# Optimization experiments

Hardware: AMD Instinct MI355X
Metric: run time of the kernel (lower is better)

## Reference

```python
import jax, jax.numpy as jnp
import numpy as np

DIM_IN, DIM_H, DIM_OUT = 1024, 512, 256
E, T, B = 8, 4, 16384


def setup_inputs() -> dict:
    key = jax.random.key(0)
    ks = jax.random.split(key, 8)
    s1 = 1.0 / np.sqrt(DIM_IN)
    s2 = 1.0 / np.sqrt(DIM_H)
    x = jax.random.normal(ks[0], (B, DIM_IN), dtype=jnp.float32)
    # stacked expert params: layer1 [E, H, IN], layer2 [E, OUT, H]
    W1 = jax.random.uniform(ks[1], (E, DIM_H, DIM_IN), jnp.float32, -s1, s1)
    b1 = jax.random.uniform(ks[2], (E, DIM_H), jnp.float32, -s1, s1)
    W2 = jax.random.uniform(ks[3], (E, DIM_OUT, DIM_H), jnp.float32, -s2, s2)
    b2 = jax.random.uniform(ks[4], (E, DIM_OUT), jnp.float32, -s2, s2)
    # gate params: [T, E, IN]
    Wg = jax.random.uniform(ks[5], (T, E, DIM_IN), jnp.float32, -s1, s1)
    bg = jax.random.uniform(ks[6], (T, E), jnp.float32, -s1, s1)
    return {"x": x, "W1": W1, "b1": b1, "W2": W2, "b2": b2, "Wg": Wg, "bg": bg}


def reference(x, W1, b1, W2, b2, Wg, bg):
    # Experts: Linear+ReLU, Linear+ReLU (dropout=0 / eval mode)
    h = jax.nn.relu(jnp.einsum('bi,ehi->beh', x, W1) + b1)          # [B,E,H]
    feats = jax.nn.relu(jnp.einsum('beh,edh->bed', h, W2) + b2)     # [B,E,D]
    # Gates: softmax over experts, one gate per task
    logits = jnp.einsum('bi,tei->bte', x, Wg) + bg                  # [B,T,E]
    w = jax.nn.softmax(logits, axis=-1)                             # [B,T,E]
    # Weighted combine: einsum('bde,be->bd') per task
    out = jnp.einsum('bed,bte->tbd', feats, w)                      # [T,B,D]
    return out
```

## Files before the change

kernel.cpp:

```cpp
#include <hip/hip_runtime.h>


typedef __attribute__((ext_vector_type(8))) __bf16 bf16x8;
typedef __attribute__((ext_vector_type(4))) float f32x4;

__device__ __forceinline__ unsigned short f2bf(float f) {
  union { float f; unsigned int i; } x;
  x.f = f;
  unsigned int r = x.i + 0x7FFFu + ((x.i >> 16) & 1u);
  return (unsigned short)(r >> 16);
}

__device__ __forceinline__ void gload_lds16(const unsigned short* g, unsigned short* l) {
  __builtin_amdgcn_global_load_lds(
      (const __attribute__((address_space(1))) void*)g,
      (__attribute__((address_space(3))) void*)l, 16, 0, 0);
}

__global__ void cvt_k(const float* __restrict__ in, unsigned short* __restrict__ out, int n4) {
  int i = blockIdx.x * blockDim.x + threadIdx.x;
  if (i >= n4) return;
  float4 v = ((const float4*)in)[i];
  ushort4 o;
  o.x = f2bf(v.x); o.y = f2bf(v.y); o.z = f2bf(v.z); o.w = f2bf(v.w);
  ((ushort4*)out)[i] = o;
}

__global__ __launch_bounds__(256) void gates_k(
    const unsigned short* __restrict__ xb,
    const unsigned short* __restrict__ Wgb,
    const float* __restrict__ bg,
    float* __restrict__ gw)
{
  const int lane = threadIdx.x & 63;
  const int wid = threadIdx.x >> 6;
  const int wgid = blockIdx.x * 4 + wid;
  const int brow = wgid * 16;
  const int l15 = lane & 15, lhi = lane >> 4;

  f32x4 acc0 = {0.f, 0.f, 0.f, 0.f};
  f32x4 acc1 = {0.f, 0.f, 0.f, 0.f};
  for (int k0 = 0; k0 < 1024; k0 += 32) {
    bf16x8 a  = *(const bf16x8*)&xb[(size_t)(brow + l15) * 1024 + k0 + lhi * 8];
    bf16x8 b0 = *(const bf16x8*)&Wgb[(size_t)l15 * 1024 + k0 + lhi * 8];
    bf16x8 b1 = *(const bf16x8*)&Wgb[(size_t)(16 + l15) * 1024 + k0 + lhi * 8];
    acc0 = __builtin_amdgcn_mfma_f32_16x16x32_bf16(a, b0, acc0, 0, 0, 0);
    acc1 = __builtin_amdgcn_mfma_f32_16x16x32_bf16(a, b1, acc1, 0, 0, 0);
  }
  const float bg0 = bg[l15];
  const float bg1 = bg[16 + l15];
#pragma unroll
  for (int r = 0; r < 4; ++r) {
    float v0 = acc0[r] + bg0;
    float v1 = acc1[r] + bg1;
    float m0 = v0, m1 = v1;
#pragma unroll
    for (int d = 1; d <= 4; d <<= 1) {
      m0 = fmaxf(m0, __shfl_xor(m0, d));
      m1 = fmaxf(m1, __shfl_xor(m1, d));
    }
    float e0 = __expf(v0 - m0), e1 = __expf(v1 - m1);
    float s0 = e0, s1 = e1;
#pragma unroll
    for (int d = 1; d <= 4; d <<= 1) {
      s0 += __shfl_xor(s0, d);
      s1 += __shfl_xor(s1, d);
    }
    int b = brow + lhi * 4 + r;
    gw[(size_t)b * 32 + l15]      = e0 / s0;
    gw[(size_t)b * 32 + 16 + l15] = e1 / s1;
  }
}

template <bool RELU>
__global__ __launch_bounds__(512, 2) void gemm256(
    const unsigned short* __restrict__ A, int lda, int aZ,
    const unsigned short* __restrict__ B,
    const float* __restrict__ bias,
    unsigned short* __restrict__ C, int ldc, int cZ,
    int tilesN, int N, int K)
{
  extern __shared__ char smem_raw[];
  unsigned short* lds = (unsigned short*)smem_raw;
  char* ldsb = (char*)smem_raw;

  const int tid = threadIdx.x;
  const int lane = tid & 63, wid = tid >> 6;
  const int wr = wid >> 2, wc = wid & 3;
  const int l15 = lane & 15, lhi = lane >> 4;

  const int nwg = gridDim.x;
  const int cpx = nwg >> 3;
  const int wg = blockIdx.x;
  const int swz = (wg & 7) * cpx + (wg >> 3);
  const int rt = swz / tilesN, ct = swz - rt * tilesN;
  const int brow = rt * 256, bcol = ct * 256;
  const int e = blockIdx.z;

  const unsigned short* Ab = A + (size_t)e * aZ + (size_t)brow * lda;
  const unsigned short* Bb = B + (size_t)e * N * K + (size_t)bcol * K;
  const float* biasb = bias + (size_t)e * N;
  unsigned short* Cb = C + (size_t)e * cZ;

  const int NT = K >> 6;
  const int NI = NT >> 1;

  const int trow = tid >> 3;
  const int cg8 = (((tid & 7) ^ (trow & 7)) << 3);

  const int axor = (l15 & 7) << 4;
  const int koff0 = (lhi << 4) ^ axor;
  const int koff1 = (64 + (lhi << 4)) ^ axor;

  const char* pA0 = ldsb + wr * 16384 + l15 * 128 + koff0;
  const char* pA1 = ldsb + wr * 16384 + l15 * 128 + koff1;
  const char* pB0 = ldsb + 65536 + wc * 8192 + l15 * 128 + koff0;
  const char* pB1 = ldsb + 65536 + wc * 8192 + l15 * 128 + koff1;

  f32x4 bias4[4];
#pragma unroll
  for (int nf = 0; nf < 4; ++nf)
    bias4[nf] = *(const f32x4*)&biasb[bcol + wc * 64 + nf * 16 + lhi * 4];

  const f32x4 zero = {0.f, 0.f, 0.f, 0.f};
  f32x4 acc[8][4];
#pragma unroll
  for (int m = 0; m < 8; ++m)
#pragma unroll
    for (int n = 0; n < 4; ++n) acc[m][n] = zero;

  auto STAGE_A = [&](int slot, int t, int u) {
    gload_lds16(Ab + (size_t)(u * 64 + trow) * lda + (t * 64 + cg8),
                lds + slot * 16384 + u * 4096 + wid * 512);
  };
  auto STAGE_B = [&](int slot, int t, int u) {
    gload_lds16(Bb + (size_t)(u * 64 + trow) * K + (t * 64 + cg8),
                lds + 32768 + slot * 16384 + u * 4096 + wid * 512);
  };

#pragma unroll
  for (int u = 0; u < 4; ++u) STAGE_B(0, 0, u);
#pragma unroll
  for (int u = 0; u < 4; ++u) STAGE_A(0, 0, u);
  asm volatile("s_waitcnt vmcnt(0)" ::: "memory");
  __builtin_amdgcn_s_barrier();

  auto ktile = [&](int slot, int tn, bool stageNext) {
    bf16x8 af[4][2], bfr[4][2];
#pragma unroll
    for (int mi = 0; mi < 4; ++mi) {
      af[mi][0] = *(const bf16x8*)(pA0 + slot * 32768 + mi * 2048);
      af[mi][1] = *(const bf16x8*)(pA1 + slot * 32768 + mi * 2048);
    }
#pragma unroll
    for (int n = 0; n < 2; ++n) {
      bfr[n][0] = *(const bf16x8*)(pB0 + slot * 32768 + n * 2048);
      bfr[n][1] = *(const bf16x8*)(pB1 + slot * 32768 + n * 2048);
    }
    if (stageNext) { STAGE_B(slot ^ 1, tn, 0); STAGE_B(slot ^ 1, tn, 1); }
    __builtin_amdgcn_s_barrier();
    __builtin_amdgcn_s_setprio(1);
#pragma unroll
    for (int kk = 0; kk < 2; ++kk)
#pragma unroll
      for (int mi = 0; mi < 4; ++mi)
#pragma unroll
        for (int n = 0; n < 2; ++n)
          acc[mi][n] = __builtin_amdgcn_mfma_f32_16x16x32_bf16(bfr[n][kk], af[mi][kk], acc[mi][n], 0, 0, 0);
    __builtin_amdgcn_s_setprio(0);
    __builtin_amdgcn_s_barrier();

#pragma unroll
    for (int n = 0; n < 2; ++n) {
      bfr[2 + n][0] = *(const bf16x8*)(pB0 + slot * 32768 + (2 + n) * 2048);
      bfr[2 + n][1] = *(const bf16x8*)(pB1 + slot * 32768 + (2 + n) * 2048);
    }
    if (stageNext) { STAGE_B(slot ^ 1, tn, 2); STAGE_B(slot ^ 1, tn, 3); }
    __builtin_amdgcn_s_barrier();
    __builtin_amdgcn_s_setprio(1);
#pragma unroll
    for (int kk = 0; kk < 2; ++kk)
#pragma unroll
      for (int mi = 0; mi < 4; ++mi)
#pragma unroll
        for (int n = 0; n < 2; ++n)
          acc[mi][2 + n] = __builtin_amdgcn_mfma_f32_16x16x32_bf16(bfr[2 + n][kk], af[mi][kk], acc[mi][2 + n], 0, 0, 0);
    __builtin_amdgcn_s_setprio(0);
    asm volatile("s_waitcnt vmcnt(4)" ::: "memory");
    __builtin_amdgcn_s_barrier();

#pragma unroll
    for (int mi = 0; mi < 4; ++mi) {
      af[mi][0] = *(const bf16x8*)(pA0 + slot * 32768 + 8192 + mi * 2048);
      af[mi][1] = *(const bf16x8*)(pA1 + slot * 32768 + 8192 + mi * 2048);
    }
    if (stageNext) { STAGE_A(slot ^ 1, tn, 0); STAGE_A(slot ^ 1, tn, 2); }
    __builtin_amdgcn_s_barrier();
    __builtin_amdgcn_s_setprio(1);
#pragma unroll
    for (int kk = 0; kk < 2; ++kk)
#pragma unroll
      for (int mi = 0; mi < 4; ++mi)
#pragma unroll
        for (int n = 0; n < 2; ++n)
          acc[4 + mi][n] = __builtin_amdgcn_mfma_f32_16x16x32_bf16(bfr[n][kk], af[mi][kk], acc[4 + mi][n], 0, 0, 0);
    __builtin_amdgcn_s_setprio(0);
    __builtin_amdgcn_s_barrier();

    if (stageNext) { STAGE_A(slot ^ 1, tn, 1); STAGE_A(slot ^ 1, tn, 3); }
    __builtin_amdgcn_s_barrier();
    __builtin_amdgcn_s_setprio(1);
#pragma unroll
    for (int kk = 0; kk < 2; ++kk)
#pragma unroll
      for (int mi = 0; mi < 4; ++mi)
#pragma unroll
        for (int n = 0; n < 2; ++n)
          acc[4 + mi][2 + n] = __builtin_amdgcn_mfma_f32_16x16x32_bf16(bfr[2 + n][kk], af[mi][kk], acc[4 + mi][2 + n], 0, 0, 0);
    __builtin_amdgcn_s_setprio(0);
    asm volatile("s_waitcnt vmcnt(2)" ::: "memory");
    __builtin_amdgcn_s_barrier();
  };

#pragma unroll 1
  for (int i = 0; i < NI; ++i) {
    ktile(0, 2 * i + 1, true);
    ktile(1, 2 * i + 2, (2 * i + 2) < NT);
  }

#pragma unroll
  for (int mf = 0; mf < 8; ++mf) {
    const size_t rowoff = (size_t)(brow + wr * 128 + mf * 16 + l15) * ldc;
#pragma unroll
    for (int nf = 0; nf < 4; ++nf) {
      const int col = bcol + wc * 64 + nf * 16 + lhi * 4;
      f32x4 v = acc[mf][nf];
      ushort4 o;
      float v0 = v[0] + bias4[nf][0];
      float v1 = v[1] + bias4[nf][1];
      float v2 = v[2] + bias4[nf][2];
      float v3 = v[3] + bias4[nf][3];
      if (RELU) {
        v0 = v0 > 0.f ? v0 : 0.f;
        v1 = v1 > 0.f ? v1 : 0.f;
        v2 = v2 > 0.f ? v2 : 0.f;
        v3 = v3 > 0.f ? v3 : 0.f;
      }
      o.x = f2bf(v0); o.y = f2bf(v1); o.z = f2bf(v2); o.w = f2bf(v3);
      *(ushort4*)&Cb[rowoff + col] = o;
    }
  }
}

__global__ __launch_bounds__(512, 4) void expert2_combine_k(
    const unsigned short* __restrict__ H,
    const unsigned short* __restrict__ W2b,
    const float* __restrict__ b2,
    const float* __restrict__ gw,
    float* __restrict__ out)
{
  __shared__ unsigned short Hs[4 * 4096];
  __shared__ float gws[32 * 65];

  const int tid = threadIdx.x;
  const int lane = tid & 63, wid = tid >> 6;
  const int wr = wid >> 2, wc = wid & 3;
  const int l15 = lane & 15, lhi = lane >> 4;
  const int brow = blockIdx.x * 64;
  const int bcol = blockIdx.y * 128;

  for (int i = tid; i < 64 * 32; i += 512) {
    int c = i & 31, r = i >> 5;
    gws[c * 65 + r] = gw[(size_t)(brow + r) * 32 + c];
  }

  const int trow = tid >> 3;
  const int cg8 = (((tid & 7) ^ (trow & 7)) << 3);
  const unsigned short* Hb = H + ((size_t)brow + trow) * 4096;
  unsigned short* HsW = Hs + wid * 512;

  const int axor = (l15 & 7) << 4;
  const char* pH = (const char*)Hs + (wr * 32 + l15) * 128;
  const int koff0 = (0 + (lhi << 4)) ^ axor;
  const int koff1 = (64 + (lhi << 4)) ^ axor;

  const size_t w2r0 = (size_t)(bcol + wc * 32 + l15) * 512;

  const f32x4 zero = {0.f, 0.f, 0.f, 0.f};
  f32x4 oacc[4][2][2];
#pragma unroll
  for (int t = 0; t < 4; ++t)
#pragma unroll
    for (int m = 0; m < 2; ++m)
#pragma unroll
      for (int n = 0; n < 2; ++n) oacc[t][m][n] = zero;

  auto STAGE = [&](int tb, int cc) {
    gload_lds16(Hb + (cc << 6) + cg8, HsW + tb * 4096);
  };

  STAGE(0, 0);
  STAGE(1, 1);
  __syncthreads();

#pragma unroll 1
  for (int e = 0; e < 8; ++e) {
    f32x4 g[2][2];
#pragma unroll
    for (int m = 0; m < 2; ++m)
#pragma unroll
      for (int n = 0; n < 2; ++n) g[m][n] = zero;

#pragma unroll
    for (int c = 0; c < 8; ++c) {
      const int cc = e * 8 + c;

      bf16x8 bfr[2][2];
#pragma unroll
      for (int n = 0; n < 2; ++n) {
        const size_t wrow = (size_t)e * 256 * 512 + w2r0 + (size_t)n * 16 * 512;
        bfr[n][0] = *(const bf16x8*)&W2b[wrow + (c << 6) + lhi * 8];
        bfr[n][1] = *(const bf16x8*)&W2b[wrow + (c << 6) + 32 + lhi * 8];
      }

      STAGE((c + 2) & 3, (cc + 2 < 64) ? (cc + 2) : 63);

      bf16x8 af[2][2];
#pragma unroll
      for (int m = 0; m < 2; ++m) {
        af[m][0] = *(const bf16x8*)(pH + ((c & 3) * 8192) + m * 2048 + koff0);
        af[m][1] = *(const bf16x8*)(pH + ((c & 3) * 8192) + m * 2048 + koff1);
      }

#pragma unroll
      for (int kk = 0; kk < 2; ++kk)
#pragma unroll
        for (int m = 0; m < 2; ++m)
#pragma unroll
          for (int n = 0; n < 2; ++n)
            g[m][n] = __builtin_amdgcn_mfma_f32_16x16x32_bf16(bfr[n][kk], af[m][kk], g[m][n], 0, 0, 0);

      if (c == 7) {
#pragma unroll
        for (int n = 0; n < 2; ++n) {
          f32x4 bv = *(const f32x4*)&b2[e * 256 + bcol + wc * 32 + n * 16 + lhi * 4];
#pragma unroll
          for (int m = 0; m < 2; ++m) {
            f32x4 v = g[m][n];
#pragma unroll
            for (int r = 0; r < 4; ++r) {
              float f = v[r] + bv[r];
              v[r] = f > 0.f ? f : 0.f;
            }
            g[m][n] = v;
          }
        }
#pragma unroll
        for (int t = 0; t < 4; ++t)
#pragma unroll
          for (int m = 0; m < 2; ++m) {
            float gwt = gws[(t * 8 + e) * 65 + wr * 32 + m * 16 + l15];
#pragma unroll
            for (int n = 0; n < 2; ++n)
#pragma unroll
              for (int r = 0; r < 4; ++r)
                oacc[t][m][n][r] += gwt * g[m][n][r];
          }
      }

      asm volatile("s_waitcnt vmcnt(1)" ::: "memory");
      __builtin_amdgcn_s_barrier();
    }
  }

  asm volatile("s_waitcnt vmcnt(0)" ::: "memory");

#pragma unroll
  for (int t = 0; t < 4; ++t)
#pragma unroll
    for (int m = 0; m < 2; ++m) {
      const size_t rowoff = ((size_t)t * 16384 + brow + wr * 32 + m * 16 + l15) * 256;
#pragma unroll
      for (int n = 0; n < 2; ++n)
        *(f32x4*)&out[rowoff + bcol + wc * 32 + n * 16 + lhi * 4] = oacc[t][m][n];
    }
}

extern "C" void kernel_launch(void* const* d_in, const int* in_sizes, int n_in,
                              void* d_out, int out_size, void* d_ws, size_t ws_size,
                              hipStream_t stream) {
  (void)in_sizes; (void)n_in; (void)out_size; (void)ws_size;
  const float* x  = (const float*)d_in[0];
  const float* W1 = (const float*)d_in[1];
  const float* b1 = (const float*)d_in[2];
  const float* W2 = (const float*)d_in[3];
  const float* b2 = (const float*)d_in[4];
  const float* Wg = (const float*)d_in[5];
  const float* bg = (const float*)d_in[6];
  float* out = (float*)d_out;

  char* ws = (char*)d_ws;
  unsigned short* xb    = (unsigned short*)ws; ws += (size_t)16384 * 1024 * 2;
  unsigned short* W1b   = (unsigned short*)ws; ws += (size_t)4096 * 1024 * 2;
  unsigned short* W2b   = (unsigned short*)ws; ws += (size_t)2048 * 512 * 2;
  unsigned short* Wgb   = (unsigned short*)ws; ws += (size_t)32 * 1024 * 2;
  float*          gw    = (float*)ws;         ws += (size_t)16384 * 32 * 4;
  unsigned short* H     = (unsigned short*)ws; ws += (size_t)16384 * 4096 * 2;

  cvt_k<<<16384, 256, 0, stream>>>(x, xb, 16384 * 1024 / 4);
  cvt_k<<<4096, 256, 0, stream>>>(W1, W1b, 4096 * 1024 / 4);
  cvt_k<<<1024, 256, 0, stream>>>(W2, W2b, 2048 * 512 / 4);
  cvt_k<<<32, 256, 0, stream>>>(Wg, Wgb, 32 * 1024 / 4);

  gates_k<<<256, 256, 0, stream>>>(xb, Wgb, bg, gw);

  gemm256<true><<<dim3(1024, 1, 1), 512, 131072, stream>>>(
      xb, 1024, 0, W1b, b1, H, 4096, 0, 16, 4096, 1024);

  expert2_combine_k<<<dim3(256, 2, 1), 512, 0, stream>>>(H, W2b, b2, gw, out);
}
```

Measured before the change: 333.9 us.

## Double-buffer W2 fragments and deepen H staging in expert2 combine kernel

Restructures the expert2_combine loop so the W2 register fragments for the next k-chunk are prefetched one step ahead into a double buffer, and the H LDS staging runs three chunks ahead instead of two. The wait/barrier moves to the top of each iteration with a looser vmcnt so global loads overlap the MFMAs. It also drops the occupancy hint from launch_bounds and switches the H and output stores to nontemporal stores. The extra prefetch registers may lower occupancy, and the hand-tuned vmcnt count must match the number of outstanding loads.

```diff
diff --git a/kernel.cpp b/kernel.cpp
--- a/kernel.cpp
+++ b/kernel.cpp
@@ -3,6 +3,7 @@
 
 typedef __attribute__((ext_vector_type(8))) __bf16 bf16x8;
 typedef __attribute__((ext_vector_type(4))) float f32x4;
+typedef __attribute__((ext_vector_type(4))) unsigned short u16x4;
 
 __device__ __forceinline__ unsigned short f2bf(float f) {
   union { float f; unsigned int i; } x;
@@ -235,7 +236,7 @@
     for (int nf = 0; nf < 4; ++nf) {
       const int col = bcol + wc * 64 + nf * 16 + lhi * 4;
       f32x4 v = acc[mf][nf];
-      ushort4 o;
+      u16x4 o;
       float v0 = v[0] + bias4[nf][0];
       float v1 = v[1] + bias4[nf][1];
       float v2 = v[2] + bias4[nf][2];
@@ -246,13 +247,13 @@
         v2 = v2 > 0.f ? v2 : 0.f;
         v3 = v3 > 0.f ? v3 : 0.f;
       }
-      o.x = f2bf(v0); o.y = f2bf(v1); o.z = f2bf(v2); o.w = f2bf(v3);
-      *(ushort4*)&Cb[rowoff + col] = o;
-    }
-  }
-}
-
-__global__ __launch_bounds__(512, 4) void expert2_combine_k(
+      o[0] = f2bf(v0); o[1] = f2bf(v1); o[2] = f2bf(v2); o[3] = f2bf(v3);
+      __builtin_nontemporal_store(o, (u16x4*)&Cb[rowoff + col]);
+    }
+  }
+}
+
+__global__ __launch_bounds__(512) void expert2_combine_k(
     const unsigned short* __restrict__ H,
     const unsigned short* __restrict__ W2b,
     const float* __restrict__ b2,
@@ -295,12 +296,25 @@
 #pragma unroll
       for (int n = 0; n < 2; ++n) oacc[t][m][n] = zero;
 
+  bf16x8 bfr[2][2][2];
+
   auto STAGE = [&](int tb, int cc) {
     gload_lds16(Hb + (cc << 6) + cg8, HsW + tb * 4096);
   };
+  auto LOADB = [&](int buf, int jn) {
+    const int en = jn >> 3, cn = jn & 7;
+#pragma unroll
+    for (int n = 0; n < 2; ++n) {
+      const size_t wrow = (size_t)en * 131072 + w2r0 + (size_t)n * 8192;
+      bfr[buf][n][0] = *(const bf16x8*)&W2b[wrow + (cn << 6) + lhi * 8];
+      bfr[buf][n][1] = *(const bf16x8*)&W2b[wrow + (cn << 6) + 32 + lhi * 8];
+    }
+  };
 
   STAGE(0, 0);
   STAGE(1, 1);
+  STAGE(2, 2);
+  LOADB(0, 0);
   __syncthreads();
 
 #pragma unroll 1
@@ -313,23 +327,29 @@
 
 #pragma unroll
     for (int c = 0; c < 8; ++c) {
-      const int cc = e * 8 + c;
-
-      bf16x8 bfr[2][2];
-#pragma unroll
-      for (int n = 0; n < 2; ++n) {
-        const size_t wrow = (size_t)e * 256 * 512 + w2r0 + (size_t)n * 16 * 512;
-        bfr[n][0] = *(const bf16x8*)&W2b[wrow + (c << 6) + lhi * 8];
-        bfr[n][1] = *(const bf16x8*)&W2b[wrow + (c << 6) + 32 + lhi * 8];
-      }
-
-      STAGE((c + 2) & 3, (cc + 2 < 64) ? (cc + 2) : 63);
+      const int j = e * 8 + c;
+
+      if (j > 0) {
+        asm volatile("s_waitcnt vmcnt(6)" ::: "memory");
+        __builtin_amdgcn_s_barrier();
+      }
+
+      {
+        int jn = j + 1; if (jn > 63) jn = 63;
+        LOADB((c + 1) & 1, jn);
+      }
+      __builtin_amdgcn_sched_barrier(0);
+
+      {
+        int js = j + 3; int cc = js > 63 ? 63 : js;
+        STAGE(js & 3, cc);
+      }
 
       bf16x8 af[2][2];
 #pragma unroll
       for (int m = 0; m < 2; ++m) {
-        af[m][0] = *(const bf16x8*)(pH + ((c & 3) * 8192) + m * 2048 + koff0);
-        af[m][1] = *(const bf16x8*)(pH + ((c & 3) * 8192) + m * 2048 + koff1);
+        af[m][0] = *(const bf16x8*)(pH + ((j & 3) * 8192) + m * 2048 + koff0);
+        af[m][1] = *(const bf16x8*)(pH + ((j & 3) * 8192) + m * 2048 + koff1);
       }
 
 #pragma unroll
@@ -338,7 +358,7 @@
         for (int m = 0; m < 2; ++m)
 #pragma unroll
           for (int n = 0; n < 2; ++n)
-            g[m][n] = __builtin_amdgcn_mfma_f32_16x16x32_bf16(bfr[n][kk], af[m][kk], g[m][n], 0, 0, 0);
+            g[m][n] = __builtin_amdgcn_mfma_f32_16x16x32_bf16(bfr[c & 1][n][kk], af[m][kk], g[m][n], 0, 0, 0);
 
       if (c == 7) {
 #pragma unroll
@@ -367,9 +387,6 @@
                 oacc[t][m][n][r] += gwt * g[m][n][r];
           }
       }
-
-      asm volatile("s_waitcnt vmcnt(1)" ::: "memory");
-      __builtin_amdgcn_s_barrier();
     }
   }
 
@@ -382,7 +399,8 @@
       const size_t rowoff = ((size_t)t * 16384 + brow + wr * 32 + m * 16 + l15) * 256;
 #pragma unroll
       for (int n = 0; n < 2; ++n)
-        *(f32x4*)&out[rowoff + bcol + wc * 32 + n * 16 + lhi * 4] = oacc[t][m][n];
+        __builtin_nontemporal_store(oacc[t][m][n],
+            (f32x4*)&out[rowoff + bcol + wc * 32 + n * 16 + lhi * 4]);
     }
 }
 
```

Result: slower. 382.5 us (+14.6%).
